# Performance work log

Hardware: AMD Instinct MI355X
Metric: run time of the kernel (lower is better)

## Reference

```python
import jax, jax.numpy as jnp
import numpy as np

B, N, E, EMB, IN = 8192, 100, 1600, 5, 1
MLP_IN = 50 * 2 * EMB + 50 * 52  # 3100


def _glorot(k, shape):
    fan_in = shape[0]
    return (jax.random.normal(k, shape, jnp.float32) / np.sqrt(fan_in)).astype(jnp.float32)


def setup_inputs() -> dict:
    key = jax.random.key(0)
    ks = jax.random.split(key, 32)
    inp = {
        "data": jax.random.normal(ks[0], (B, N, IN), jnp.float32),
        "d": jax.random.normal(ks[1], (B, 50, 52), jnp.float32),
        "src": jax.random.randint(ks[2], (E,), 0, N, jnp.int32),
        "dst": jax.random.randint(ks[3], (E,), 0, N, jnp.int32),
    }
    # 3 GatedRGCN layers: (1->5), (5->5), (5->5); each has a feature linear W,b and a gate linear G,gb
    dims = [(IN, EMB), (EMB, EMB), (EMB, EMB)]
    for i, (fi, fo) in enumerate(dims):
        inp[f"W{i}"] = _glorot(ks[4 + 4 * i], (fi, fo))
        inp[f"b{i}"] = jnp.zeros((fo,), jnp.float32)
        inp[f"G{i}"] = _glorot(ks[5 + 4 * i], (fo, fo))
        inp[f"gb{i}"] = jnp.zeros((fo,), jnp.float32)
    # MLP head: 3100 -> 128 -> 128 -> 64 -> 2
    mdims = [(MLP_IN, 128), (128, 128), (128, 64), (64, 2)]
    for i, (fi, fo) in enumerate(mdims):
        inp[f"F{i + 1}"] = _glorot(ks[16 + 2 * i], (fi, fo))
        inp[f"fb{i + 1}"] = jnp.zeros((fo,), jnp.float32)
    return inp


def _gated_rgcn_layer(h, src, dst, W, b, G, gb):
    # h: [B, N, F_in]; sum-aggregate neighbor features along edges, then gated linear.
    msgs = h[:, src, :]                                   # [B, E, F_in] gather
    agg = jnp.zeros_like(h).at[:, dst, :].add(msgs)       # [B, N, F_in] scatter-add
    h2 = agg @ W + b                                      # [B, N, F_out]
    gate = jax.nn.sigmoid(h2 @ G + gb)                    # elementwise edge-free gate
    return jax.nn.leaky_relu(gate * h2)                   # LeakyReLU(0.01), torch default


def reference(data, d, src, dst,
              W0, b0, G0, gb0, W1, b1, G1, gb1, W2, b2, G2, gb2,
              F1, fb1, F2, fb2, F3, fb3, F4, fb4):
    x = data
    x = _gated_rgcn_layer(x, src, dst, W0, b0, G0, gb0)
    x = _gated_rgcn_layer(x, src, dst, W1, b1, G1, gb1)
    x = _gated_rgcn_layer(x, src, dst, W2, b2, G2, gb2)
    x = x.reshape(x.shape[0], -1)                         # [B, 500]
    x = jnp.concatenate([x, d.reshape(d.shape[0], -1)], axis=1)  # [B, 3100]
    x = jax.nn.leaky_relu(x @ F1 + fb1)
    x = jax.nn.leaky_relu(x @ F2 + fb2)
    x = jax.nn.leaky_relu(x @ F3 + fb3)
    x = jax.nn.sigmoid(x @ F4 + fb4)                      # [B, 2]
    return x
```

## Files before the change

### kernel.cpp

```cpp
#include <hip/hip_runtime.h>
#include <math.h>

#define NT 256
#define NTG 1024
constexpr int B_   = 8192;
constexpr int N_   = 100;
constexpr int E_   = 1600;
constexpr int EMB  = 5;
constexpr int XDIM = 500;
constexpr int DDIM = 2600;
constexpr int XWP  = 512;
constexpr int DOFF = 512;
constexpr int KPAD = 3136;
constexpr int NKC  = 98;
constexpr int H1 = 128, H2 = 128, H3 = 64, HO = 2;

typedef short short8 __attribute__((ext_vector_type(8)));
typedef float f32x4  __attribute__((ext_vector_type(4)));

__device__ __forceinline__ float leaky(float v) { return v > 0.f ? v : 0.01f * v; }
__device__ __forceinline__ float sigm(float v)  { return 1.f / (1.f + __expf(-v)); }
__device__ __forceinline__ unsigned short f2bf(float f) {
  unsigned int x = __float_as_uint(f);
  return (unsigned short)((x + 0x7fffu + ((x >> 16) & 1u)) >> 16);
}


__global__ __launch_bounds__(NT) void setup_kernel(
    const int* __restrict__ src, const int* __restrict__ dst,
    int* __restrict__ off_g, int* __restrict__ lst_g,
    const float* __restrict__ F1, const float* __restrict__ F2, const float* __restrict__ F3,
    unsigned short* __restrict__ F1c, unsigned short* __restrict__ F2T, unsigned short* __restrict__ F3T,
    const float* __restrict__ dmat, unsigned short* __restrict__ awf)
{
  const int blk = blockIdx.x;
  const int t   = threadIdx.x;

  if (blk == 0) {
    __shared__ int cnt[N_ + 1];
    __shared__ int cur[N_];
    if (t <= N_) cnt[t] = 0;
    __syncthreads();
    for (int e = t; e < E_; e += NT) atomicAdd(&cnt[dst[e] + 1], 1);
    __syncthreads();
    if (t == 0) {
      int s = 0;
      for (int n = 0; n <= N_; ++n) { s += cnt[n]; cnt[n] = s; }
    }
    __syncthreads();
    if (t < N_) cur[t] = cnt[t];
    if (t <= N_) off_g[t] = cnt[t];
    __syncthreads();
    for (int e = t; e < E_; e += NT) {
      int d = dst[e];
      int p = atomicAdd(&cur[d], 1);
      lst_g[p] = src[e];
    }
  } else if (blk <= 320) {
    const int b = blk - 1;
    if (b < 128) {
      for (int k = t; k < KPAD; k += NT) {
        float v = 0.f;
        if (k < XDIM)                          v = F1[(size_t)k * H1 + b];
        else if (k >= DOFF && k < DOFF + DDIM) v = F1[(size_t)(k - DOFF + XDIM) * H1 + b];
        int kc = k >> 5, q = (k >> 3) & 3, e = k & 7;
        int lane = (b & 15) + q * 16;
        F1c[((size_t)(b >> 4) * NKC + kc) * 512 + lane * 8 + e] = f2bf(v);
      }
    } else if (b < 256) {
      int n = b - 128;
      if (t < 128) F2T[n * 128 + t] = f2bf(F2[(size_t)t * H2 + n]);
    } else {
      int n = b - 256;
      if (n < 64 && t < 128) F3T[n * 128 + t] = f2bf(F3[(size_t)t * H3 + n]);
    }
  } else {
    const int R = blk - 321;
    __shared__ __attribute__((aligned(16))) unsigned short tile[16][520];
    const float* dbase = dmat + (size_t)R * 16 * DDIM;
    for (int ct = 0; ct < 6; ++ct) {
      const int c0 = ct * 512;
      if (ct == 5) {
        for (int i = t; i < 16 * 520; i += NT) ((unsigned short*)tile)[i] = 0;
        __syncthreads();
      }
      const int nc4 = (ct < 5) ? 128 : 10;
      for (int i = t; i < 16 * nc4; i += NT) {
        int r = i / nc4, c4 = i - r * nc4;
        float4 f = *(const float4*)(dbase + (size_t)r * DDIM + c0 + c4 * 4);
        unsigned short* tp = &tile[r][c4 * 4];
        tp[0] = (unsigned short)(__float_as_uint(f.x) >> 16);
        tp[1] = (unsigned short)(__float_as_uint(f.y) >> 16);
        tp[2] = (unsigned short)(__float_as_uint(f.z) >> 16);
        tp[3] = (unsigned short)(__float_as_uint(f.w) >> 16);
      }
      __syncthreads();
      const int nkc = (ct < 5) ? 16 : 2;
      for (int i = t; i < nkc * 64; i += NT) {
        int kcL = i >> 6, lane = i & 63;
        int r = lane & 15, q = lane >> 4;
        uint4 p = *(const uint4*)&tile[r][kcL * 32 + q * 8];
        ((uint4*)awf)[((size_t)R * NKC + 16 + ct * 16 + kcL) * 64 + lane] = p;
      }
      __syncthreads();
    }
  }
}

constexpr int BT2 = 32;

__device__ __forceinline__ void rgcn_layer(
    const float* __restrict__ RB, float* __restrict__ WB,
    const float* __restrict__ wts, const int* __restrict__ soff,
    const int* __restrict__ sl160, int t, int wof)
{
  if (t < N_ * (BT2 / 4)) {
    const int n  = t >> 3;
    const int b4 = (t & 7) * 4;
    f32x4 a[5];
#pragma unroll
    for (int j = 0; j < 5; ++j) a[j] = (f32x4){0.f, 0.f, 0.f, 0.f};
    const int qe = soff[n + 1];
    for (int q = soff[n]; q < qe; ++q) {
      const float* base = RB + sl160[q] + b4;
#pragma unroll
      for (int j = 0; j < 5; ++j) a[j] += *(const f32x4*)(base + j * 32);
    }
    f32x4 h2[5];
#pragma unroll
    for (int j = 0; j < 5; ++j) {
      float bb = wts[wof + 25 + j];
      f32x4 v = (f32x4){bb, bb, bb, bb};
#pragma unroll
      for (int k = 0; k < 5; ++k) v += a[k] * wts[wof + k * 5 + j];
      h2[j] = v;
    }
#pragma unroll
    for (int j = 0; j < 5; ++j) {
      float gb = wts[wof + 55 + j];
      f32x4 g = (f32x4){gb, gb, gb, gb};
#pragma unroll
      for (int k = 0; k < 5; ++k) g += h2[k] * wts[wof + 30 + k * 5 + j];
      f32x4 o;
#pragma unroll
      for (int c = 0; c < 4; ++c) o[c] = leaky(sigm(g[c]) * h2[j][c]);
      *(f32x4*)(WB + n * 160 + j * 32 + b4) = o;
    }
  }
}

__global__ __launch_bounds__(NTG) void gnn_kernel(
    const float* __restrict__ data,
    const int* __restrict__ off_g, const int* __restrict__ lst_g,
    const float* __restrict__ W0, const float* __restrict__ b0, const float* __restrict__ G0, const float* __restrict__ gb0,
    const float* __restrict__ W1, const float* __restrict__ b1, const float* __restrict__ G1, const float* __restrict__ gb1,
    const float* __restrict__ W2, const float* __restrict__ b2, const float* __restrict__ G2, const float* __restrict__ gb2,
    unsigned short* __restrict__ awf)
{
  __shared__ __attribute__((aligned(16))) float bufA[BT2 * 513];
  __shared__ __attribute__((aligned(16))) float bufB[XDIM * BT2];
  __shared__ int   soff[N_ + 1];
  __shared__ int   sl160[E_];
  __shared__ float wts[160];
  const int t   = threadIdx.x;
  const int b0_ = blockIdx.x * BT2;

  for (int i = t; i < E_; i += NTG) sl160[i] = lst_g[i] * 160;
  if (t <= N_) soff[t] = off_g[t];
  if (t < 5)  { wts[t] = W0[t]; wts[5 + t] = b0[t]; wts[35 + t] = gb0[t]; }
  if (t < 25) { wts[10 + t] = G0[t];
                wts[40 + t] = W1[t]; wts[70 + t]  = G1[t];
                wts[100 + t] = W2[t]; wts[130 + t] = G2[t]; }
  if (t < 5)  { wts[65 + t] = b1[t]; wts[95 + t]  = gb1[t];
                wts[125 + t] = b2[t]; wts[155 + t] = gb2[t]; }
  for (int i = t; i < N_ * BT2; i += NTG) {
    int b = i / N_, n = i - b * N_;
    bufA[n * 160 + b] = data[(size_t)b0_ * N_ + i];
  }
  __syncthreads();

  if (t < N_ * (BT2 / 4)) {
    const int n  = t >> 3;
    const int b4 = (t & 7) * 4;
    f32x4 a = (f32x4){0.f, 0.f, 0.f, 0.f};
    const int qe = soff[n + 1];
    for (int q = soff[n]; q < qe; ++q) a += *(const f32x4*)(bufA + sl160[q] + b4);
    f32x4 h2[5];
#pragma unroll
    for (int j = 0; j < 5; ++j) {
      float bb = wts[5 + j];
      h2[j] = a * wts[j] + (f32x4){bb, bb, bb, bb};
    }
#pragma unroll
    for (int j = 0; j < 5; ++j) {
      float gb = wts[35 + j];
      f32x4 g = (f32x4){gb, gb, gb, gb};
#pragma unroll
      for (int k = 0; k < 5; ++k) g += h2[k] * wts[10 + k * 5 + j];
      f32x4 o;
#pragma unroll
      for (int c = 0; c < 4; ++c) o[c] = leaky(sigm(g[c]) * h2[j][c]);
      *(f32x4*)(bufB + n * 160 + j * 32 + b4) = o;
    }
  }
  __syncthreads();

  rgcn_layer(bufB, bufA, wts, soff, sl160, t, 40);
  __syncthreads();
  rgcn_layer(bufA, bufB, wts, soff, sl160, t, 100);
  __syncthreads();

  for (int i = t; i < BT2 * XWP; i += NTG) {
    int b = i & 31, r = i >> 5;
    bufA[b * 513 + r] = (r < XDIM) ? bufB[r * 32 + b] : 0.f;
  }
  __syncthreads();

  {
    const int R0 = blockIdx.x * 2;
    for (int i = t; i < 32 * 64; i += NTG) {
      int f = i >> 6, lane = i & 63;
      int h = f >> 4, kc = f & 15;
      int b = h * 16 + (lane & 15);
      int k0 = kc * 32 + (lane >> 4) * 8;
      const float* sp = bufA + b * 513 + k0;
      uint4 p;
      p.x = (unsigned)f2bf(sp[0]) | ((unsigned)f2bf(sp[1]) << 16);
      p.y = (unsigned)f2bf(sp[2]) | ((unsigned)f2bf(sp[3]) << 16);
      p.z = (unsigned)f2bf(sp[4]) | ((unsigned)f2bf(sp[5]) << 16);
      p.w = (unsigned)f2bf(sp[6]) | ((unsigned)f2bf(sp[7]) << 16);
      ((uint4*)awf)[((size_t)(R0 + h) * NKC + kc) * 64 + lane] = p;
    }
  }
}

constexpr int MBG = 32;
constexpr int MB2 = 16;
constexpr int EST = 136;
constexpr int KSPLIT = 7;
constexpr int SCC = 7;

__global__ __launch_bounds__(NT, 4) void mlp_main(
    const unsigned short* __restrict__ awf,
    const unsigned short* __restrict__ F1c, float* __restrict__ part)
{
  const int t     = threadIdx.x;
  const int rb    = blockIdx.x & 255;
  const int split = blockIdx.x >> 8;
  const int row0  = rb * MBG;
  const int lane  = t & 63;
  const int w     = t >> 6;
  const int quad  = lane >> 4;
  const int ln    = lane & 15;
  const int kc0   = split * (2 * SCC);

  const unsigned short* a0p = awf + (((size_t)(rb * 2 + 0) * NKC + kc0) * 64 + lane) * 8;
  const unsigned short* a1p = awf + (((size_t)(rb * 2 + 1) * NKC + kc0) * 64 + lane) * 8;
  const unsigned short* b0p = F1c + (((size_t)(w * 2 + 0) * NKC + kc0) * 64 + lane) * 8;
  const unsigned short* b1p = F1c + (((size_t)(w * 2 + 1) * NKC + kc0) * 64 + lane) * 8;

#define LOADF(Ax, Bx, c)                                                       \
  {                                                                            \
    _Pragma("unroll")                                                          \
    for (int s_ = 0; s_ < 2; ++s_) {                                           \
      const int o_ = (2 * (c) + s_) * 512;                                     \
      Ax[s_][0] = *(const short8*)(a0p + o_);                                  \
      Ax[s_][1] = *(const short8*)(a1p + o_);                                  \
      Bx[s_][0] = *(const short8*)(b0p + o_);                                  \
      Bx[s_][1] = *(const short8*)(b1p + o_);                                  \
    }                                                                          \
  }

  f32x4 a00 = {0.f, 0.f, 0.f, 0.f};
  f32x4 a01 = {0.f, 0.f, 0.f, 0.f};
  f32x4 a10 = {0.f, 0.f, 0.f, 0.f};
  f32x4 a11 = {0.f, 0.f, 0.f, 0.f};
  short8 A0[2][2], A1[2][2], B0[2][2], B1[2][2];

  LOADF(A0, B0, 0)
  LOADF(A1, B1, 1)
  for (int c = 0; c < SCC; ++c) {
    if (c & 1) {
#pragma unroll
      for (int s = 0; s < 2; ++s) {
        a00 = __builtin_amdgcn_mfma_f32_16x16x32_bf16(A1[s][0], B1[s][0], a00, 0, 0, 0);
        a01 = __builtin_amdgcn_mfma_f32_16x16x32_bf16(A1[s][0], B1[s][1], a01, 0, 0, 0);
        a10 = __builtin_amdgcn_mfma_f32_16x16x32_bf16(A1[s][1], B1[s][0], a10, 0, 0, 0);
        a11 = __builtin_amdgcn_mfma_f32_16x16x32_bf16(A1[s][1], B1[s][1], a11, 0, 0, 0);
      }
      if (c + 2 < SCC) LOADF(A1, B1, c + 2)
    } else {
#pragma unroll
      for (int s = 0; s < 2; ++s) {
        a00 = __builtin_amdgcn_mfma_f32_16x16x32_bf16(A0[s][0], B0[s][0], a00, 0, 0, 0);
        a01 = __builtin_amdgcn_mfma_f32_16x16x32_bf16(A0[s][0], B0[s][1], a01, 0, 0, 0);
        a10 = __builtin_amdgcn_mfma_f32_16x16x32_bf16(A0[s][1], B0[s][0], a10, 0, 0, 0);
        a11 = __builtin_amdgcn_mfma_f32_16x16x32_bf16(A0[s][1], B0[s][1], a11, 0, 0, 0);
      }
      if (c + 2 < SCC) LOADF(A0, B0, c + 2)
    }
  }
#undef LOADF

  const int col0 = w * 32 + ln;
  float* pp = part + ((size_t)split * B_ + row0) * H1;
#pragma unroll
  for (int r = 0; r < 4; ++r) {
    int m = quad * 4 + r;
    pp[m * H1 + col0]             = a00[r];
    pp[m * H1 + col0 + 16]        = a01[r];
    pp[(m + 16) * H1 + col0]      = a10[r];
    pp[(m + 16) * H1 + col0 + 16] = a11[r];
  }
}

__global__ __launch_bounds__(NT) void tail_kernel(
    const float* __restrict__ part, const float* __restrict__ fb1,
    const unsigned short* __restrict__ F2T, const float* __restrict__ fb2,
    const unsigned short* __restrict__ F3T, const float* __restrict__ fb3,
    const float* __restrict__ F4, const float* __restrict__ fb4,
    float* __restrict__ out)
{
  __shared__ __attribute__((aligned(16))) unsigned short sH[MB2 * EST];
  __shared__ float sh3[MB2 * 68];

  const int t    = threadIdx.x;
  const int row0 = blockIdx.x * MB2;
  const int lane = t & 63;
  const int w    = t >> 6;
  const int quad = lane >> 4;
  const int ln   = lane & 15;
  const int q8   = quad * 8;
  constexpr size_t PS = (size_t)B_ * H1;

  for (int i = t; i < MB2 * H1; i += NT) {
    int m = i >> 7, col = i & 127;
    size_t off = (size_t)(row0 + m) * H1 + col;
    float v = fb1[col];
#pragma unroll
    for (int s = 0; s < KSPLIT; ++s) v += part[s * PS + off];
    sH[m * EST + col] = f2bf(leaky(v));
  }
  __syncthreads();

  const int col0 = w * 32 + ln;
  f32x4 a20 = {0.f, 0.f, 0.f, 0.f};
  f32x4 a21 = {0.f, 0.f, 0.f, 0.f};
  {
    const unsigned short* g2a = F2T + (size_t)col0 * H2 + q8;
    const unsigned short* g2b = g2a + (size_t)16 * H2;
#pragma unroll
    for (int s = 0; s < 4; ++s) {
      short8 b0f = *(const short8*)(g2a + s * 32);
      short8 b1f = *(const short8*)(g2b + s * 32);
      short8 af  = *(const short8*)(sH + ln * EST + s * 32 + q8);
      a20 = __builtin_amdgcn_mfma_f32_16x16x32_bf16(af, b0f, a20, 0, 0, 0);
      a21 = __builtin_amdgcn_mfma_f32_16x16x32_bf16(af, b1f, a21, 0, 0, 0);
    }
  }
  __syncthreads();
  {
    float bb0 = fb2[col0], bb1 = fb2[col0 + 16];
#pragma unroll
    for (int r = 0; r < 4; ++r) {
      int m = quad * 4 + r;
      sH[m * EST + col0]      = f2bf(leaky(a20[r] + bb0));
      sH[m * EST + col0 + 16] = f2bf(leaky(a21[r] + bb1));
    }
  }
  __syncthreads();

  f32x4 a3 = {0.f, 0.f, 0.f, 0.f};
  {
    const unsigned short* g3 = F3T + (size_t)(w * 16 + ln) * H2 + q8;
#pragma unroll
    for (int s = 0; s < 4; ++s) {
      short8 bf = *(const short8*)(g3 + s * 32);
      short8 af = *(const short8*)(sH + ln * EST + s * 32 + q8);
      a3 = __builtin_amdgcn_mfma_f32_16x16x32_bf16(af, bf, a3, 0, 0, 0);
    }
  }
  {
    int col = w * 16 + ln;
    float bb = fb3[col];
#pragma unroll
    for (int r = 0; r < 4; ++r)
      sh3[(quad * 4 + r) * 68 + col] = leaky(a3[r] + bb);
  }
  __syncthreads();

  if (t < MB2 * HO) {
    int m = t >> 1, j = t & 1;
    float a = fb4[j];
#pragma unroll 8
    for (int k = 0; k < H3; ++k) a += sh3[m * 68 + k] * F4[k * HO + j];
    out[(size_t)(row0 + m) * HO + j] = sigm(a);
  }
}

extern "C" void kernel_launch(void* const* d_in, const int* in_sizes, int n_in,
                              void* d_out, int out_size, void* d_ws, size_t ws_size,
                              hipStream_t stream) {
  const float* data = (const float*)d_in[0];
  const float* dmat = (const float*)d_in[1];
  const int*   src  = (const int*)d_in[2];
  const int*   dst  = (const int*)d_in[3];
  const float* W0 = (const float*)d_in[4];  const float* b0 = (const float*)d_in[5];
  const float* G0 = (const float*)d_in[6];  const float* gb0 = (const float*)d_in[7];
  const float* W1 = (const float*)d_in[8];  const float* b1 = (const float*)d_in[9];
  const float* G1 = (const float*)d_in[10]; const float* gb1 = (const float*)d_in[11];
  const float* W2 = (const float*)d_in[12]; const float* b2 = (const float*)d_in[13];
  const float* G2 = (const float*)d_in[14]; const float* gb2 = (const float*)d_in[15];
  const float* F1 = (const float*)d_in[16]; const float* fb1 = (const float*)d_in[17];
  const float* F2 = (const float*)d_in[18]; const float* fb2 = (const float*)d_in[19];
  const float* F3 = (const float*)d_in[20]; const float* fb3 = (const float*)d_in[21];
  const float* F4 = (const float*)d_in[22]; const float* fb4 = (const float*)d_in[23];
  float* out = (float*)d_out;

  unsigned short* awf = (unsigned short*)d_ws;
  unsigned short* F1c = awf + (size_t)B_ * KPAD;
  unsigned short* F2T = F1c + 128 * KPAD;
  unsigned short* F3T = F2T + 128 * 128;
  int* off_g = (int*)(F3T + 64 * 128);
  int* lst_g = off_g + 104;
  float* part = (float*)(lst_g + 1600);

  setup_kernel<<<1 + 320 + 512, NT, 0, stream>>>(src, dst, off_g, lst_g,
                                                 F1, F2, F3, F1c, F2T, F3T,
                                                 dmat, awf);
  gnn_kernel<<<B_ / BT2, NTG, 0, stream>>>(data, off_g, lst_g,
                                           W0, b0, G0, gb0,
                                           W1, b1, G1, gb1,
                                           W2, b2, G2, gb2, awf);
  mlp_main<<<(B_ / MBG) * KSPLIT, NT, 0, stream>>>(awf, F1c, part);
  tail_kernel<<<B_ / MB2, NT, 0, stream>>>(part, fb1, F2T, fb2,
                                           F3T, fb3, F4, fb4, out);
}
```

Before: 253.6 us.

## Fuse d-matrix conversion, first MLP layer and tail into one kernel

The setup kernel no longer converts the d matrix into the bf16 fragment buffer. The new fused MLP kernel streams d rows directly from global memory into a shared tile, converts them on the fly, and runs the whole first-layer K loop plus layers 2-4 per 16-row block. This removes the split-K partial-sum buffer, the separate tail kernel, and the large intermediate writes and reads of the converted d matrix. In exchange, each block now handles the full K range with a single accumulator per wave, which gives less per-wave parallelism and adds shared-memory syncs.

Measured after the change: 341.0 us. +34.5%, slower.

```diff
diff --git a/kernel.cpp b/kernel.cpp
--- a/kernel.cpp
+++ b/kernel.cpp
@@ -13,7 +13,9 @@
 constexpr int DOFF = 512;
 constexpr int KPAD = 3136;
 constexpr int NKC  = 98;
+constexpr int XKC  = 16;
 constexpr int H1 = 128, H2 = 128, H3 = 64, HO = 2;
+constexpr int EST = 136;
 
 typedef short short8 __attribute__((ext_vector_type(8)));
 typedef float f32x4  __attribute__((ext_vector_type(4)));
@@ -30,8 +32,7 @@
     const int* __restrict__ src, const int* __restrict__ dst,
     int* __restrict__ off_g, int* __restrict__ lst_g,
     const float* __restrict__ F1, const float* __restrict__ F2, const float* __restrict__ F3,
-    unsigned short* __restrict__ F1c, unsigned short* __restrict__ F2T, unsigned short* __restrict__ F3T,
-    const float* __restrict__ dmat, unsigned short* __restrict__ awf)
+    unsigned short* __restrict__ F1c, unsigned short* __restrict__ F2T, unsigned short* __restrict__ F3T)
 {
   const int blk = blockIdx.x;
   const int t   = threadIdx.x;
@@ -56,7 +57,7 @@
       int p = atomicAdd(&cur[d], 1);
       lst_g[p] = src[e];
     }
-  } else if (blk <= 320) {
+  } else {
     const int b = blk - 1;
     if (b < 128) {
       for (int k = t; k < KPAD; k += NT) {
@@ -74,36 +75,6 @@
       int n = b - 256;
       if (n < 64 && t < 128) F3T[n * 128 + t] = f2bf(F3[(size_t)t * H3 + n]);
     }
-  } else {
-    const int R = blk - 321;
-    __shared__ __attribute__((aligned(16))) unsigned short tile[16][520];
-    const float* dbase = dmat + (size_t)R * 16 * DDIM;
-    for (int ct = 0; ct < 6; ++ct) {
-      const int c0 = ct * 512;
-      if (ct == 5) {
-        for (int i = t; i < 16 * 520; i += NT) ((unsigned short*)tile)[i] = 0;
-        __syncthreads();
-      }
-      const int nc4 = (ct < 5) ? 128 : 10;
-      for (int i = t; i < 16 * nc4; i += NT) {
-        int r = i / nc4, c4 = i - r * nc4;
-        float4 f = *(const float4*)(dbase + (size_t)r * DDIM + c0 + c4 * 4);
-        unsigned short* tp = &tile[r][c4 * 4];
-        tp[0] = (unsigned short)(__float_as_uint(f.x) >> 16);
-        tp[1] = (unsigned short)(__float_as_uint(f.y) >> 16);
-        tp[2] = (unsigned short)(__float_as_uint(f.z) >> 16);
-        tp[3] = (unsigned short)(__float_as_uint(f.w) >> 16);
-      }
-      __syncthreads();
-      const int nkc = (ct < 5) ? 16 : 2;
-      for (int i = t; i < nkc * 64; i += NT) {
-        int kcL = i >> 6, lane = i & 63;
-        int r = lane & 15, q = lane >> 4;
-        uint4 p = *(const uint4*)&tile[r][kcL * 32 + q * 8];
-        ((uint4*)awf)[((size_t)R * NKC + 16 + ct * 16 + kcL) * 64 + lane] = p;
-      }
-      __syncthreads();
-    }
   }
 }
 
@@ -229,167 +200,169 @@
       p.y = (unsigned)f2bf(sp[2]) | ((unsigned)f2bf(sp[3]) << 16);
       p.z = (unsigned)f2bf(sp[4]) | ((unsigned)f2bf(sp[5]) << 16);
       p.w = (unsigned)f2bf(sp[6]) | ((unsigned)f2bf(sp[7]) << 16);
-      ((uint4*)awf)[((size_t)(R0 + h) * NKC + kc) * 64 + lane] = p;
-    }
-  }
-}
-
-constexpr int MBG = 32;
-constexpr int MB2 = 16;
-constexpr int EST = 136;
-constexpr int KSPLIT = 7;
-constexpr int SCC = 7;
-
-__global__ __launch_bounds__(NT, 4) void mlp_main(
+      ((uint4*)awf)[((size_t)(R0 + h) * XKC + kc) * 64 + lane] = p;
+    }
+  }
+}
+
+__global__ __launch_bounds__(512, 4) void mlp_fused(
     const unsigned short* __restrict__ awf,
-    const unsigned short* __restrict__ F1c, float* __restrict__ part)
-{
-  const int t     = threadIdx.x;
-  const int rb    = blockIdx.x & 255;
-  const int split = blockIdx.x >> 8;
-  const int row0  = rb * MBG;
-  const int lane  = t & 63;
-  const int w     = t >> 6;
-  const int quad  = lane >> 4;
-  const int ln    = lane & 15;
-  const int kc0   = split * (2 * SCC);
-
-  const unsigned short* a0p = awf + (((size_t)(rb * 2 + 0) * NKC + kc0) * 64 + lane) * 8;
-  const unsigned short* a1p = awf + (((size_t)(rb * 2 + 1) * NKC + kc0) * 64 + lane) * 8;
-  const unsigned short* b0p = F1c + (((size_t)(w * 2 + 0) * NKC + kc0) * 64 + lane) * 8;
-  const unsigned short* b1p = F1c + (((size_t)(w * 2 + 1) * NKC + kc0) * 64 + lane) * 8;
-
-#define LOADF(Ax, Bx, c)                                                       \
-  {                                                                            \
-    _Pragma("unroll")                                                          \
-    for (int s_ = 0; s_ < 2; ++s_) {                                           \
-      const int o_ = (2 * (c) + s_) * 512;                                     \
-      Ax[s_][0] = *(const short8*)(a0p + o_);                                  \
-      Ax[s_][1] = *(const short8*)(a1p + o_);                                  \
-      Bx[s_][0] = *(const short8*)(b0p + o_);                                  \
-      Bx[s_][1] = *(const short8*)(b1p + o_);                                  \
-    }                                                                          \
-  }
-
-  f32x4 a00 = {0.f, 0.f, 0.f, 0.f};
-  f32x4 a01 = {0.f, 0.f, 0.f, 0.f};
-  f32x4 a10 = {0.f, 0.f, 0.f, 0.f};
-  f32x4 a11 = {0.f, 0.f, 0.f, 0.f};
-  short8 A0[2][2], A1[2][2], B0[2][2], B1[2][2];
-
-  LOADF(A0, B0, 0)
-  LOADF(A1, B1, 1)
-  for (int c = 0; c < SCC; ++c) {
-    if (c & 1) {
-#pragma unroll
-      for (int s = 0; s < 2; ++s) {
-        a00 = __builtin_amdgcn_mfma_f32_16x16x32_bf16(A1[s][0], B1[s][0], a00, 0, 0, 0);
-        a01 = __builtin_amdgcn_mfma_f32_16x16x32_bf16(A1[s][0], B1[s][1], a01, 0, 0, 0);
-        a10 = __builtin_amdgcn_mfma_f32_16x16x32_bf16(A1[s][1], B1[s][0], a10, 0, 0, 0);
-        a11 = __builtin_amdgcn_mfma_f32_16x16x32_bf16(A1[s][1], B1[s][1], a11, 0, 0, 0);
-      }
-      if (c + 2 < SCC) LOADF(A1, B1, c + 2)
-    } else {
-#pragma unroll
-      for (int s = 0; s < 2; ++s) {
-        a00 = __builtin_amdgcn_mfma_f32_16x16x32_bf16(A0[s][0], B0[s][0], a00, 0, 0, 0);
-        a01 = __builtin_amdgcn_mfma_f32_16x16x32_bf16(A0[s][0], B0[s][1], a01, 0, 0, 0);
-        a10 = __builtin_amdgcn_mfma_f32_16x16x32_bf16(A0[s][1], B0[s][0], a10, 0, 0, 0);
-        a11 = __builtin_amdgcn_mfma_f32_16x16x32_bf16(A0[s][1], B0[s][1], a11, 0, 0, 0);
-      }
-      if (c + 2 < SCC) LOADF(A0, B0, c + 2)
-    }
-  }
-#undef LOADF
-
-  const int col0 = w * 32 + ln;
-  float* pp = part + ((size_t)split * B_ + row0) * H1;
-#pragma unroll
-  for (int r = 0; r < 4; ++r) {
-    int m = quad * 4 + r;
-    pp[m * H1 + col0]             = a00[r];
-    pp[m * H1 + col0 + 16]        = a01[r];
-    pp[(m + 16) * H1 + col0]      = a10[r];
-    pp[(m + 16) * H1 + col0 + 16] = a11[r];
-  }
-}
-
-__global__ __launch_bounds__(NT) void tail_kernel(
-    const float* __restrict__ part, const float* __restrict__ fb1,
+    const unsigned short* __restrict__ F1c,
+    const float* __restrict__ dmat,
+    const float* __restrict__ fb1,
     const unsigned short* __restrict__ F2T, const float* __restrict__ fb2,
     const unsigned short* __restrict__ F3T, const float* __restrict__ fb3,
     const float* __restrict__ F4, const float* __restrict__ fb4,
     float* __restrict__ out)
 {
-  __shared__ __attribute__((aligned(16))) unsigned short sH[MB2 * EST];
-  __shared__ float sh3[MB2 * 68];
+  __shared__ __attribute__((aligned(16))) unsigned short tile[16][520];
+  __shared__ __attribute__((aligned(16))) unsigned short sH[16 * EST];
+  __shared__ float sh3[16 * 68];
 
   const int t    = threadIdx.x;
-  const int row0 = blockIdx.x * MB2;
+  const int rb   = blockIdx.x;
+  const int row0 = rb * 16;
   const int lane = t & 63;
   const int w    = t >> 6;
-  const int quad = lane >> 4;
-  const int ln   = lane & 15;
-  const int q8   = quad * 8;
-  constexpr size_t PS = (size_t)B_ * H1;
-
-  for (int i = t; i < MB2 * H1; i += NT) {
-    int m = i >> 7, col = i & 127;
-    size_t off = (size_t)(row0 + m) * H1 + col;
-    float v = fb1[col];
-#pragma unroll
-    for (int s = 0; s < KSPLIT; ++s) v += part[s * PS + off];
-    sH[m * EST + col] = f2bf(leaky(v));
-  }
-  __syncthreads();
-
-  const int col0 = w * 32 + ln;
-  f32x4 a20 = {0.f, 0.f, 0.f, 0.f};
-  f32x4 a21 = {0.f, 0.f, 0.f, 0.f};
+  const int r    = lane & 15;
+  const int q    = lane >> 4;
+  const int q8   = q * 8;
+
+  const unsigned short* ap = awf + (size_t)rb * XKC * 512 + lane * 8;
+  const unsigned short* bp = F1c + (size_t)w * NKC * 512 + lane * 8;
+  const float* dbase = dmat + (size_t)row0 * DDIM;
+
+  f32x4 acc = {0.f, 0.f, 0.f, 0.f};
+  short8 Ar[2], Br[2];
+  float4 sv[4];
+
+  Ar[0] = *(const short8*)(ap);
+  Ar[1] = *(const short8*)(ap + 512);
+  Br[0] = *(const short8*)(bp);
+  Br[1] = *(const short8*)(bp + 512);
+#pragma unroll
+  for (int i = 0; i < 4; ++i) {
+    int e = i * 512 + t, rr = e >> 7, cc = e & 127;
+    sv[i] = *(const float4*)(dbase + (size_t)rr * DDIM + cc * 4);
+  }
+  for (int kc = 0; kc < 16; ++kc) {
+    int cur = kc & 1;
+    short8 a = Ar[cur], b = Br[cur];
+    if (kc < 14) Ar[cur] = *(const short8*)(ap + (kc + 2) * 512);
+    Br[cur] = *(const short8*)(bp + (kc + 2) * 512);
+    acc = __builtin_amdgcn_mfma_f32_16x16x32_bf16(a, b, acc, 0, 0, 0);
+  }
+#pragma unroll
+  for (int i = 0; i < 4; ++i) {
+    int e = i * 512 + t, rr = e >> 7, cc = e & 127;
+    uint2 p;
+    p.x = (__float_as_uint(sv[i].y) & 0xffff0000u) | (__float_as_uint(sv[i].x) >> 16);
+    p.y = (__float_as_uint(sv[i].w) & 0xffff0000u) | (__float_as_uint(sv[i].z) >> 16);
+    *(uint2*)&tile[rr][cc * 4] = p;
+  }
+  __syncthreads();
+
+  const unsigned short* tb = &tile[r][q8];
+  for (int ct = 0; ct < 6; ++ct) {
+    const int nk   = (ct < 5) ? 16 : 2;
+    const int kcg0 = 16 + ct * 16;
+    if (ct < 4) {
+#pragma unroll
+      for (int i = 0; i < 4; ++i) {
+        int e = i * 512 + t, rr = e >> 7, cc = e & 127;
+        sv[i] = *(const float4*)(dbase + (size_t)rr * DDIM + (ct + 1) * 512 + cc * 4);
+      }
+    } else if (ct == 4) {
+      if (t < 160) {
+        int rr = t / 10, cc = t % 10;
+        sv[0] = *(const float4*)(dbase + (size_t)rr * DDIM + 2560 + cc * 4);
+      }
+    }
+    short8 Dr[2];
+    Dr[0] = *(const short8*)(tb);
+    Dr[1] = *(const short8*)(tb + 32);
+    for (int kcL = 0; kcL < nk; ++kcL) {
+      int kc  = kcg0 + kcL;
+      int cur = kcL & 1;
+      short8 a = Dr[cur], b = Br[kc & 1];
+      if (kcL + 2 < nk)  Dr[cur]    = *(const short8*)(tb + (kcL + 2) * 32);
+      if (kc + 2 < NKC)  Br[kc & 1] = *(const short8*)(bp + (kc + 2) * 512);
+      acc = __builtin_amdgcn_mfma_f32_16x16x32_bf16(a, b, acc, 0, 0, 0);
+    }
+    if (ct == 5) break;
+    __syncthreads();
+    if (ct < 4) {
+#pragma unroll
+      for (int i = 0; i < 4; ++i) {
+        int e = i * 512 + t, rr = e >> 7, cc = e & 127;
+        uint2 p;
+        p.x = (__float_as_uint(sv[i].y) & 0xffff0000u) | (__float_as_uint(sv[i].x) >> 16);
+        p.y = (__float_as_uint(sv[i].w) & 0xffff0000u) | (__float_as_uint(sv[i].z) >> 16);
+        *(uint2*)&tile[rr][cc * 4] = p;
+      }
+    } else {
+      if (t < 160) {
+        int rr = t / 10, cc = t % 10;
+        uint2 p;
+        p.x = (__float_as_uint(sv[0].y) & 0xffff0000u) | (__float_as_uint(sv[0].x) >> 16);
+        p.y = (__float_as_uint(sv[0].w) & 0xffff0000u) | (__float_as_uint(sv[0].z) >> 16);
+        *(uint2*)&tile[rr][cc * 4] = p;
+      } else if (t < 256) {
+        int idx = t - 160, r2 = idx / 6, c2 = 40 + (idx % 6) * 4;
+        *(uint2*)&tile[r2][c2] = make_uint2(0u, 0u);
+      }
+    }
+    __syncthreads();
+  }
+
   {
-    const unsigned short* g2a = F2T + (size_t)col0 * H2 + q8;
-    const unsigned short* g2b = g2a + (size_t)16 * H2;
+    float b1v = fb1[w * 16 + r];
+#pragma unroll
+    for (int reg = 0; reg < 4; ++reg) {
+      int m = q * 4 + reg;
+      sH[m * EST + w * 16 + r] = f2bf(leaky(acc[reg] + b1v));
+    }
+  }
+  __syncthreads();
+
+  f32x4 a2 = {0.f, 0.f, 0.f, 0.f};
+  {
+    const unsigned short* g2 = F2T + (size_t)(w * 16 + r) * H2 + q8;
 #pragma unroll
     for (int s = 0; s < 4; ++s) {
-      short8 b0f = *(const short8*)(g2a + s * 32);
-      short8 b1f = *(const short8*)(g2b + s * 32);
-      short8 af  = *(const short8*)(sH + ln * EST + s * 32 + q8);
-      a20 = __builtin_amdgcn_mfma_f32_16x16x32_bf16(af, b0f, a20, 0, 0, 0);
-      a21 = __builtin_amdgcn_mfma_f32_16x16x32_bf16(af, b1f, a21, 0, 0, 0);
+      short8 bf = *(const short8*)(g2 + s * 32);
+      short8 af = *(const short8*)(sH + r * EST + s * 32 + q8);
+      a2 = __builtin_amdgcn_mfma_f32_16x16x32_bf16(af, bf, a2, 0, 0, 0);
     }
   }
   __syncthreads();
   {
-    float bb0 = fb2[col0], bb1 = fb2[col0 + 16];
-#pragma unroll
-    for (int r = 0; r < 4; ++r) {
-      int m = quad * 4 + r;
-      sH[m * EST + col0]      = f2bf(leaky(a20[r] + bb0));
-      sH[m * EST + col0 + 16] = f2bf(leaky(a21[r] + bb1));
-    }
-  }
-  __syncthreads();
-
-  f32x4 a3 = {0.f, 0.f, 0.f, 0.f};
-  {
-    const unsigned short* g3 = F3T + (size_t)(w * 16 + ln) * H2 + q8;
+    float b2v = fb2[w * 16 + r];
+#pragma unroll
+    for (int reg = 0; reg < 4; ++reg) {
+      int m = q * 4 + reg;
+      sH[m * EST + w * 16 + r] = f2bf(leaky(a2[reg] + b2v));
+    }
+  }
+  __syncthreads();
+
+  if (w < 4) {
+    f32x4 a3 = {0.f, 0.f, 0.f, 0.f};
+    const unsigned short* g3 = F3T + (size_t)(w * 16 + r) * H2 + q8;
 #pragma unroll
     for (int s = 0; s < 4; ++s) {
       short8 bf = *(const short8*)(g3 + s * 32);
-      short8 af = *(const short8*)(sH + ln * EST + s * 32 + q8);
+      short8 af = *(const short8*)(sH + r * EST + s * 32 + q8);
       a3 = __builtin_amdgcn_mfma_f32_16x16x32_bf16(af, bf, a3, 0, 0, 0);
     }
-  }
-  {
-    int col = w * 16 + ln;
-    float bb = fb3[col];
-#pragma unroll
-    for (int r = 0; r < 4; ++r)
-      sh3[(quad * 4 + r) * 68 + col] = leaky(a3[r] + bb);
-  }
-  __syncthreads();
-
-  if (t < MB2 * HO) {
+    float b3v = fb3[w * 16 + r];
+#pragma unroll
+    for (int reg = 0; reg < 4; ++reg)
+      sh3[(q * 4 + reg) * 68 + w * 16 + r] = leaky(a3[reg] + b3v);
+  }
+  __syncthreads();
+
+  if (t < 16 * HO) {
     int m = t >> 1, j = t & 1;
     float a = fb4[j];
 #pragma unroll 8
@@ -418,21 +391,18 @@
   float* out = (float*)d_out;
 
   unsigned short* awf = (unsigned short*)d_ws;
-  unsigned short* F1c = awf + (size_t)B_ * KPAD;
+  unsigned short* F1c = awf + (size_t)(B_ / 16) * XKC * 512;
   unsigned short* F2T = F1c + 128 * KPAD;
   unsigned short* F3T = F2T + 128 * 128;
   int* off_g = (int*)(F3T + 64 * 128);
   int* lst_g = off_g + 104;
-  float* part = (float*)(lst_g + 1600);
-
-  setup_kernel<<<1 + 320 + 512, NT, 0, stream>>>(src, dst, off_g, lst_g,
-                                                 F1, F2, F3, F1c, F2T, F3T,
-                                                 dmat, awf);
+
+  setup_kernel<<<321, NT, 0, stream>>>(src, dst, off_g, lst_g,
+                                       F1, F2, F3, F1c, F2T, F3T);
   gnn_kernel<<<B_ / BT2, NTG, 0, stream>>>(data, off_g, lst_g,
                                            W0, b0, G0, gb0,
                                            W1, b1, G1, gb1,
                                            W2, b2, G2, gb2, awf);
-  mlp_main<<<(B_ / MBG) * KSPLIT, NT, 0, stream>>>(awf, F1c, part);
-  tail_kernel<<<B_ / MB2, NT, 0, stream>>>(part, fb1, F2T, fb2,
-                                           F3T, fb3, F4, fb4, out);
-}
+  mlp_fused<<<B_ / 16, 512, 0, stream>>>(awf, F1c, dmat, fb1, F2T, fb2,
+                                         F3T, fb3, F4, fb4, out);
+}
```
